# Optimization experiments

Hardware: AMD Instinct MI355X
Metric: run time of the kernel (lower is better)

Reference implementation:

```python
import jax, jax.numpy as jnp
import numpy as np

HEADS = 6
WSIZE = 8
SHIFTS = 4
EPS = 1e-5


def conv1x1(x, w, b=None):
    # x: (B,C,H,W), w: (O,C)
    y = jnp.einsum('bchw,oc->bohw', x, w)
    if b is not None:
        y = y + b[None, :, None, None]
    return y


def spatial_shift(x):
    # ShiftConv2d1 depthwise fixed-kernel conv == per-group spatial shift with zero pad
    C = x.shape[1]
    g = C // 5
    x0, x1, x2, x3, x4 = (x[:, :g], x[:, g:2 * g], x[:, 2 * g:3 * g],
                          x[:, 3 * g:4 * g], x[:, 4 * g:])
    left = jnp.pad(x0[:, :, :, 1:], ((0, 0), (0, 0), (0, 0), (0, 1)))   # kernel (1,2)
    right = jnp.pad(x1[:, :, :, :-1], ((0, 0), (0, 0), (0, 0), (1, 0)))  # kernel (1,0)
    up = jnp.pad(x2[:, :, 1:, :], ((0, 0), (0, 0), (0, 1), (0, 0)))      # kernel (2,1)
    down = jnp.pad(x3[:, :, :-1, :], ((0, 0), (0, 0), (1, 0), (0, 0)))   # kernel (0,1)
    return jnp.concatenate([left, right, up, down, x4], axis=1)


def window_attn(xb, ws, heads, shifts):
    # xb: (B, 2*heads*c, H, W); self-similarity attention q@q^T (no separate K, no scaling)
    if shifts > 0:
        xb = jnp.roll(xb, (-(ws // 2), -(ws // 2)), axis=(2, 3))
    b, c2, H, W = xb.shape
    cd = c2 // (2 * heads)
    nh, nw = H // ws, W // ws
    t = xb.reshape(b, 2, heads, cd, nh, ws, nw, ws)
    t = t.transpose(1, 0, 4, 6, 2, 5, 7, 3).reshape(2, b * nh * nw, heads, ws * ws, cd)
    q, v = t[0], t[1]
    atn = jax.nn.softmax(jnp.einsum('whnc,whmc->whnm', q, q), axis=-1)
    o = jnp.einsum('whnm,whmc->whnc', atn, v)
    o = o.reshape(b, nh, nw, heads, ws, ws, cd)
    o = o.transpose(0, 3, 6, 1, 4, 2, 5).reshape(b, heads * cd, H, W)
    if shifts > 0:
        o = jnp.roll(o, (ws // 2, ws // 2), axis=(2, 3))
    return o


def setup_inputs() -> dict:
    key = jax.random.key(0)
    ks = jax.random.split(key, 8)
    B, C, H, W = 2, 180, 256, 256
    s = 0.05
    return {
        'x': jax.random.normal(ks[0], (B, C, H, W), jnp.float32),
        'w0': jax.random.normal(ks[1], (2 * C, C), jnp.float32) * s,
        'b0': jnp.zeros((2 * C,), jnp.float32),
        'w1': jax.random.normal(ks[2], (C, 2 * C), jnp.float32) * s,
        'b1': jnp.zeros((C,), jnp.float32),
        'w_in': jax.random.normal(ks[3], (2 * C, C), jnp.float32) * s,
        'b_in': jnp.zeros((2 * C,), jnp.float32),
        'bn_g': jnp.ones((2 * C,), jnp.float32),
        'bn_b': jnp.zeros((2 * C,), jnp.float32),
        'w_out': jax.random.normal(ks[4], (C, C), jnp.float32) * s,
        'b_out': jnp.zeros((C,), jnp.float32),
    }


def reference(x, w0, b0, w1, b1, w_in, b_in, bn_g, bn_b, w_out, b_out):
    # --- LFE (shift-conv FFN), exp_ratio=2, relu ---
    y = conv1x1(spatial_shift(x), w0, b0)
    y = jax.nn.relu(y)
    y = conv1x1(spatial_shift(y), w1, b1)
    x = y + x
    # --- GMSA (3 parallel shifted-window self-similarity attentions) ---
    z = conv1x1(x, w_in, b_in)
    mu = z.mean(axis=(0, 2, 3), keepdims=True)
    var = z.var(axis=(0, 2, 3), keepdims=True)  # biased, matching BN training forward
    z = (z - mu) / jnp.sqrt(var + EPS) * bn_g[None, :, None, None] + bn_b[None, :, None, None]
    cs = z.shape[1] // 3
    sizes = [WSIZE // 4, WSIZE // 2, WSIZE]
    outs = [window_attn(z[:, i * cs:(i + 1) * cs], sizes[i], HEADS, SHIFTS)
            for i in range(3)]
    out = conv1x1(jnp.concatenate(outs, axis=1), w_out, b_out)
    return out + x
```

## Files before the change

### kernel.cpp

```cpp
#include <hip/hip_runtime.h>
#include <hip/hip_bf16.h>

#define HWSZ 65536
#define NPIX 131072

typedef unsigned short u16;
typedef __bf16 bf16x8 __attribute__((ext_vector_type(8)));
typedef float f32x4 __attribute__((ext_vector_type(4)));
typedef unsigned short u16x2 __attribute__((ext_vector_type(2)));
typedef unsigned short u16x4 __attribute__((ext_vector_type(4)));
typedef unsigned short u16x8 __attribute__((ext_vector_type(8)));
typedef unsigned short u16x8u __attribute__((ext_vector_type(8), aligned(4)));

__device__ inline u16 f2bf(float f) {
    unsigned int x = __builtin_bit_cast(unsigned int, f);
    unsigned int r = x + 0x7FFFu + ((x >> 16) & 1u);
    return (u16)(r >> 16);
}
__device__ inline float bf2f(u16 u) {
    unsigned int x = ((unsigned int)u) << 16;
    return __builtin_bit_cast(float, x);
}

__global__ __launch_bounds__(256) void prep_w(
    const float* __restrict__ w0, const float* __restrict__ w1,
    const float* __restrict__ wi, const float* __restrict__ wo,
    u16* __restrict__ W0p, u16* __restrict__ W1p,
    u16* __restrict__ Wip, u16* __restrict__ Wop)
{
    const int i = blockIdx.x * 256 + threadIdx.x;
    {
        const int r = i / 192, c = i % 192;
        const bool ok = (r < 360) && (c < 180);
        W0p[i] = ok ? f2bf(w0[r * 180 + c]) : (u16)0;
        Wip[i] = ok ? f2bf(wi[r * 180 + c]) : (u16)0;
    }
    {
        const int r = i / 384, c = i % 384;
        W1p[i] = (r < 180 && c < 360) ? f2bf(w1[r * 360 + c]) : (u16)0;
    }
    if (i < 36864) {
        const int r = i / 192, c = i % 192;
        Wop[i] = (r < 180 && c < 180) ? f2bf(wo[r * 180 + c]) : (u16)0;
    }
}

template<int CI, int G, int INM, int XSTR, bool RELU, bool BNPART>
__global__ __launch_bounds__(512) void conv_v14(
    const void* __restrict__ Xv, const u16* __restrict__ Wp,
    const float* __restrict__ bias, u16* __restrict__ Yh,
    float* __restrict__ part)
{
    constexpr int CI_PAD = ((CI + 31) / 32) * 32;
    constexpr int NSTEP  = CI_PAD / 32;
    constexpr int LDK    = 40;

    __shared__ u16 Xt[2][64 * LDK];

    const int tid = threadIdx.x;
    const int p0   = blockIdx.x << 6;
    const int b    = p0 >> 16;
    const int pix0 = p0 & 65535;
    const int h    = pix0 >> 8;
    const int w0c  = pix0 & 255;
    const int lane = tid & 63, wid = tid >> 6;
    const int lr = lane & 15, lg = lane >> 4;
    const int co_wave = wid * 48;

    const float* Xf = (const float*)Xv + (size_t)b * CI * HWSZ;
    const u16*   Xh = (const u16*)Xv;

    const int xn  = tid & 63;
    const int k4a = tid >> 6;

    auto loadX = [&](int kt, u16x4& r) {
        const int c0 = kt + k4a * 4;
        u16x4 v = {0, 0, 0, 0};
        if (c0 < CI) {
            int dh = 0, dw = 0;
            if (G > 0) {
                const int g = c0 / G;
                if      (g == 0) dw = 1;
                else if (g == 1) dw = -1;
                else if (g == 2) dh = 1;
                else if (g == 3) dh = -1;
            }
            const int hh = h + dh;
            const int wp = w0c + xn + dw;
            if (hh >= 0 && hh < 256 && wp >= 0 && wp < 256) {
                if constexpr (INM == 1) {
                    v = *(const u16x4*)&Xh[(size_t)((b << 16) | (hh << 8) | wp) * XSTR + c0];
                } else {
                    const float* xs = Xf + (size_t)c0 * HWSZ + hh * 256 + wp;
                    #pragma unroll
                    for (int j = 0; j < 4; ++j) v[j] = f2bf(xs[(size_t)j * HWSZ]);
                }
            }
        }
        r = v;
    };

    auto loadW = [&](int kt, bf16x8 (&a)[3]) {
        #pragma unroll
        for (int mf = 0; mf < 3; ++mf)
            a[mf] = *(const bf16x8*)&Wp[(size_t)(co_wave + mf * 16 + lr) * CI_PAD + kt + lg * 8];
    };

    auto writeLDS = [&](u16x4& r, int buf) {
        *(u16x4*)&Xt[buf][xn * LDK + k4a * 4] = r;
    };

    f32x4 acc[3][4] = {};
    u16x4 raw[2];
    bf16x8 af[2][3];

    loadX(0, raw[0]);
    loadW(0, af[0]);
    writeLDS(raw[0], 0);

    #pragma unroll
    for (int s = 0; s < NSTEP; ++s) {
        const int cur = s & 1, nxt = cur ^ 1;
        __syncthreads();
        if (s + 1 < NSTEP) {
            loadX((s + 1) * 32, raw[nxt]);
            loadW((s + 1) * 32, af[nxt]);
        }
        bf16x8 bfr[4];
        #pragma unroll
        for (int nf = 0; nf < 4; ++nf)
            bfr[nf] = *(const bf16x8*)&Xt[cur][(nf * 16 + lr) * LDK + lg * 8];
        #pragma unroll
        for (int mf = 0; mf < 3; ++mf)
            #pragma unroll
            for (int nf = 0; nf < 4; ++nf)
                acc[mf][nf] = __builtin_amdgcn_mfma_f32_16x16x32_bf16(
                    af[cur][mf], bfr[nf], acc[mf][nf], 0, 0, 0);
        if (s + 1 < NSTEP) writeLDS(raw[nxt], nxt);
    }

    float bsum[3][4] = {}, bsq[3][4] = {};
    #pragma unroll
    for (int mf = 0; mf < 3; ++mf) {
        const int co_b = co_wave + mf * 16 + lg * 4;
        if (co_b >= 360) continue;
        #pragma unroll
        for (int nf = 0; nf < 4; ++nf) {
            const size_t pg = (size_t)p0 + nf * 16 + lr;
            u16x4 o;
            #pragma unroll
            for (int r = 0; r < 4; ++r) {
                float v = acc[mf][nf][r] + bias[co_b + r];
                if (RELU) v = fmaxf(v, 0.f);
                o[r] = f2bf(v);
                if (BNPART) {
                    const float vr = bf2f(o[r]);
                    bsum[mf][r] += vr;
                    bsq[mf][r]  += vr * vr;
                }
            }
            *(u16x4*)&Yh[pg * 360 + co_b] = o;
        }
    }

    if (BNPART) {
        #pragma unroll
        for (int mf = 0; mf < 3; ++mf)
            #pragma unroll
            for (int r = 0; r < 4; ++r) {
                #pragma unroll
                for (int m = 1; m < 16; m <<= 1) {
                    bsum[mf][r] += __shfl_xor(bsum[mf][r], m, 64);
                    bsq[mf][r]  += __shfl_xor(bsq[mf][r],  m, 64);
                }
            }
        if (lr == 0) {
            float* pb = part + (size_t)blockIdx.x * 768;
            #pragma unroll
            for (int mf = 0; mf < 3; ++mf) {
                const int co_b = co_wave + mf * 16 + lg * 4;
                if (co_b >= 360) continue;
                f32x4 s4, q4;
                #pragma unroll
                for (int r = 0; r < 4; ++r) { s4[r] = bsum[mf][r]; q4[r] = bsq[mf][r]; }
                *(f32x4*)&pb[co_b]       = s4;
                *(f32x4*)&pb[384 + co_b] = q4;
            }
        }
    }
}

__global__ __launch_bounds__(256) void bn_fin2(const float* __restrict__ part,
                                               const float* __restrict__ g,
                                               const float* __restrict__ bb,
                                               float* __restrict__ sc,
                                               float* __restrict__ sh)
{
    const int c = blockIdx.x;
    const int t = threadIdx.x;
    float s = 0.f, q = 0.f;
    for (int k = t; k < 2048; k += 256) {
        s += part[(size_t)k * 768 + c];
        q += part[(size_t)k * 768 + 384 + c];
    }
    for (int m = 32; m; m >>= 1) {
        s += __shfl_xor(s, m, 64);
        q += __shfl_xor(q, m, 64);
    }
    __shared__ float rs[4], rq[4];
    if ((t & 63) == 0) { rs[t >> 6] = s; rq[t >> 6] = q; }
    __syncthreads();
    if (t == 0) {
        const float su = rs[0] + rs[1] + rs[2] + rs[3];
        const float sq = rq[0] + rq[1] + rq[2] + rq[3];
        const float invN = 1.f / (float)NPIX;
        const float mean = su * invN;
        const float var  = sq * invN - mean * mean;
        const float istd = 1.f / sqrtf(var + 1e-5f);
        const float scv  = g[c] * istd;
        sc[c] = scv;
        sh[c] = bb[c] - mean * scv;
    }
}

template<int CI, int CO, int G, int XSTR, bool RELU, int RES, int OUTM, int OSTR, bool COSPLIT>
__global__ __launch_bounds__(256) void conv_v10(
    const u16* __restrict__ Xh, const u16* __restrict__ Wp,
    const float* __restrict__ bias, const void* __restrict__ Rv,
    void* __restrict__ Yv)
{
    constexpr int CI_PAD = ((CI + 31) / 32) * 32;
    constexpr int NSTEP  = CI_PAD / 32;

    __shared__ u16 Xt[2][256 * 8];

    const int tid = threadIdx.x;
    const int bid = blockIdx.x;
    int px_tile, co0;
    if (COSPLIT) {
        co0     = ((bid >> 3) & 1) * 192;
        px_tile = ((bid >> 4) << 3) | (bid & 7);
    } else {
        co0 = blockIdx.y * 192; px_tile = bid;
    }
    const int p0   = px_tile << 6;
    const int b    = p0 >> 16;
    const int pix0 = p0 & 65535;
    const int h    = pix0 >> 8;
    const int w0c  = pix0 & 255;
    const int lane = tid & 63, wid = tid >> 6;
    const int lr = lane & 15, lg = lane >> 4;
    const int co_wave = co0 + wid * 48;

    const int sg  = (wid << 6) | lane;
    const int spx = sg >> 2;
    const int khp = sg & 3;
    const int kh  = khp ^ ((spx >> 1) & 3);

    auto stage = [&](int kt, int buf) {
        const int c0 = kt + kh * 8;
        u16* ldst_lane = &Xt[buf][sg * 8];
        int dh = 0, dw = 0; bool uni = true;
        if (G > 0) {
            const int g0 = c0 / G;
            uni = (g0 == (c0 + 7) / G);
            if      (g0 == 0) dw = 1;
            else if (g0 == 1) dw = -1;
            else if (g0 == 2) dh = 1;
            else if (g0 == 3) dh = -1;
        }
        const int hh = h + dh, wp = w0c + spx + dw;
        const bool pxok = (hh >= 0 && hh < 256 && wp >= 0 && wp < 256);
        if (c0 < CI && uni && pxok) {
            const u16* src = &Xh[(size_t)((b << 16) | (hh << 8) | wp) * XSTR + c0];
            u16* wbase = &Xt[buf][(wid << 6) * 8];
            __builtin_amdgcn_global_load_lds(
                (const __attribute__((address_space(1))) unsigned int*)src,
                (__attribute__((address_space(3))) unsigned int*)wbase, 16, 0, 0);
        } else {
            u16x8 t = {0, 0, 0, 0, 0, 0, 0, 0};
            if (c0 < CI && pxok) {
                #pragma unroll
                for (int j = 0; j < 8; ++j) {
                    const int c = c0 + j;
                    if (c < CI) {
                        int dh2 = 0, dw2 = 0;
                        if (G > 0) {
                            const int g = c / G;
                            if      (g == 0) dw2 = 1;
                            else if (g == 1) dw2 = -1;
                            else if (g == 2) dh2 = 1;
                            else if (g == 3) dh2 = -1;
                        }
                        const int h2 = h + dh2, w2 = w0c + spx + dw2;
                        if (h2 >= 0 && h2 < 256 && w2 >= 0 && w2 < 256)
                            t[j] = Xh[(size_t)((b << 16) | (h2 << 8) | w2) * XSTR + c];
                    }
                }
            }
            *(u16x8*)ldst_lane = t;
        }
    };

    auto loadW = [&](int kt, bf16x8 (&a)[3]) {
        #pragma unroll
        for (int mf = 0; mf < 3; ++mf)
            a[mf] = *(const bf16x8*)&Wp[(size_t)(co_wave + mf * 16 + lr) * CI_PAD + kt + lg * 8];
    };

    f32x4 acc[3][4] = {};
    bf16x8 af[2][3];

    stage(0, 0);
    loadW(0, af[0]);
    __syncthreads();

    #pragma unroll
    for (int s = 0; s < NSTEP; ++s) {
        const int cur = s & 1, nxt = cur ^ 1;
        if (s + 1 < NSTEP) {
            stage((s + 1) * 32, nxt);
            loadW((s + 1) * 32, af[nxt]);
        }
        bf16x8 bfr[4];
        #pragma unroll
        for (int nf = 0; nf < 4; ++nf) {
            const int pxr = nf * 16 + lr;
            const int kpp = lg ^ ((pxr >> 1) & 3);
            bfr[nf] = *(const bf16x8*)&Xt[cur][pxr * 32 + kpp * 8];
        }
        #pragma unroll
        for (int mf = 0; mf < 3; ++mf)
            #pragma unroll
            for (int nf = 0; nf < 4; ++nf)
                acc[mf][nf] = __builtin_amdgcn_mfma_f32_16x16x32_bf16(
                    af[cur][mf], bfr[nf], acc[mf][nf], 0, 0, 0);
        __syncthreads();
    }

    const float* Rf = (const float*)Rv;
    const u16*   Rh = (const u16*)Rv;
    #pragma unroll
    for (int mf = 0; mf < 3; ++mf) {
        const int co_b = co_wave + mf * 16 + lg * 4;
        if (co_b >= CO) continue;
        #pragma unroll
        for (int nf = 0; nf < 4; ++nf) {
            const int pl = pix0 + nf * 16 + lr;
            const size_t pg = (size_t)p0 + nf * 16 + lr;
            float v[4];
            #pragma unroll
            for (int r = 0; r < 4; ++r) {
                v[r] = acc[mf][nf][r] + bias[co_b + r];
                if (RELU) v[r] = fmaxf(v[r], 0.f);
            }
            if (RES == 1) {
                #pragma unroll
                for (int r = 0; r < 4; ++r)
                    v[r] += Rf[((size_t)(b * CO + co_b + r)) * HWSZ + pl];
            }
            if (RES == 2) {
                u16x4 rr = *(const u16x4*)&Rh[pg * 180 + co_b];
                #pragma unroll
                for (int r = 0; r < 4; ++r) v[r] += bf2f(rr[r]);
            }
            if (OUTM == 1) {
                u16x4 o;
                #pragma unroll
                for (int r = 0; r < 4; ++r) o[r] = f2bf(v[r]);
                *(u16x4*)&((u16*)Yv)[pg * OSTR + co_b] = o;
            } else {
                #pragma unroll
                for (int r = 0; r < 4; ++r)
                    ((float*)Yv)[((size_t)(b * CO + co_b + r)) * HWSZ + pl] = v[r];
            }
        }
    }
}

template<int WS>
__global__ __launch_bounds__(256) void attn_v3(
    const u16* __restrict__ zt, const float* __restrict__ scale,
    const float* __restrict__ shiftc, u16* __restrict__ ot, int chunk)
{
    constexpr int NP  = WS * WS;
    constexpr int GPB = 256 / NP;
    constexpr int SH  = WS / 2;
    constexpr int NW  = 256 / WS;

    __shared__ float qs[256 * 12];
    __shared__ float vs[256 * 12];
    __shared__ float scs[120], shs[120];

    const int tid = threadIdx.x;
    if (tid < 120) {
        scs[tid] = scale[chunk * 120 + tid];
        shs[tid] = shiftc[chunk * 120 + tid];
    }

    const int lg  = tid / NP;
    const int n   = tid % NP;
    const int gidx = blockIdx.x * GPB + lg;

    const int head = gidx % 6;
    const int win  = gidx / 6;
    const int wcol = win % NW;
    const int tmp  = win / NW;
    const int wrow = tmp % NW;
    const int b    = tmp / NW;

    const int i = n / WS, j = n % WS;
    const int hh = (wrow * WS + i + SH) & 255;
    const int ww = (wcol * WS + j + SH) & 255;
    const size_t zrow = (size_t)((b << 16) | (hh << 8) | ww) * 360;

    const int cq = chunk * 120 + head * 10;
    const int cl = head * 10;

    u16x8u q8 = *(const u16x8u*)&zt[zrow + cq];
    u16x2  q2 = *(const u16x2*)&zt[zrow + cq + 8];
    u16x8u v8 = *(const u16x8u*)&zt[zrow + cq + 60];
    u16x2  v2 = *(const u16x2*)&zt[zrow + cq + 68];
    __syncthreads();

    float q[10];
    float* qrow = &qs[tid * 12];
    float* vrow = &vs[tid * 12];
    #pragma unroll
    for (int c = 0; c < 8; ++c) {
        q[c] = bf2f(q8[c]) * scs[cl + c] + shs[cl + c];
        qrow[c] = q[c];
        vrow[c] = bf2f(v8[c]) * scs[60 + cl + c] + shs[60 + cl + c];
    }
    q[8] = bf2f(q2[0]) * scs[cl + 8] + shs[cl + 8];
    q[9] = bf2f(q2[1]) * scs[cl + 9] + shs[cl + 9];
    qrow[8] = q[8]; qrow[9] = q[9];
    vrow[8] = bf2f(v2[0]) * scs[60 + cl + 8] + shs[60 + cl + 8];
    vrow[9] = bf2f(v2[1]) * scs[60 + cl + 9] + shs[60 + cl + 9];
    qrow[10] = 0.f; qrow[11] = 0.f;
    vrow[10] = 0.f; vrow[11] = 0.f;
    __syncthreads();

    const float* qg = &qs[(lg * NP) * 12];
    const float* vg = &vs[(lg * NP) * 12];

    float mx = -1e30f;
    for (int m = 0; m < NP; ++m) {
        f32x4 a0 = *(const f32x4*)&qg[m * 12];
        f32x4 a1 = *(const f32x4*)&qg[m * 12 + 4];
        f32x4 a2 = *(const f32x4*)&qg[m * 12 + 8];
        float d = q[0]*a0[0] + q[1]*a0[1] + q[2]*a0[2] + q[3]*a0[3]
                + q[4]*a1[0] + q[5]*a1[1] + q[6]*a1[2] + q[7]*a1[3]
                + q[8]*a2[0] + q[9]*a2[1];
        mx = fmaxf(mx, d);
    }
    float s = 0.f;
    float o[10] = {};
    for (int m = 0; m < NP; ++m) {
        f32x4 a0 = *(const f32x4*)&qg[m * 12];
        f32x4 a1 = *(const f32x4*)&qg[m * 12 + 4];
        f32x4 a2 = *(const f32x4*)&qg[m * 12 + 8];
        float d = q[0]*a0[0] + q[1]*a0[1] + q[2]*a0[2] + q[3]*a0[3]
                + q[4]*a1[0] + q[5]*a1[1] + q[6]*a1[2] + q[7]*a1[3]
                + q[8]*a2[0] + q[9]*a2[1];
        float e = __expf(d - mx);
        s += e;
        f32x4 b0 = *(const f32x4*)&vg[m * 12];
        f32x4 b1 = *(const f32x4*)&vg[m * 12 + 4];
        f32x4 b2 = *(const f32x4*)&vg[m * 12 + 8];
        o[0] += e * b0[0]; o[1] += e * b0[1]; o[2] += e * b0[2]; o[3] += e * b0[3];
        o[4] += e * b1[0]; o[5] += e * b1[1]; o[6] += e * b1[2]; o[7] += e * b1[3];
        o[8] += e * b2[0]; o[9] += e * b2[1];
    }
    const float inv = 1.f / s;
    u16* orow = ot + (size_t)((b << 16) | (hh << 8) | ww) * 180 + chunk * 60 + head * 10;
    u16x8u o8;
    #pragma unroll
    for (int c = 0; c < 8; ++c) o8[c] = f2bf(o[c] * inv);
    u16x2 o2;
    o2[0] = f2bf(o[8] * inv);
    o2[1] = f2bf(o[9] * inv);
    *(u16x8u*)&orow[0] = o8;
    *(u16x2*)&orow[8]  = o2;
}

extern "C" void kernel_launch(void* const* d_in, const int* in_sizes, int n_in,
                              void* d_out, int out_size, void* d_ws, size_t ws_size,
                              hipStream_t stream)
{
    const float* x     = (const float*)d_in[0];
    const float* w0    = (const float*)d_in[1];
    const float* b0    = (const float*)d_in[2];
    const float* w1    = (const float*)d_in[3];
    const float* b1    = (const float*)d_in[4];
    const float* w_in  = (const float*)d_in[5];
    const float* b_in  = (const float*)d_in[6];
    const float* bn_g  = (const float*)d_in[7];
    const float* bn_b  = (const float*)d_in[8];
    const float* w_out = (const float*)d_in[9];
    const float* b_out = (const float*)d_in[10];
    float* out = (float*)d_out;

    u16* y   = (u16*)d_ws;
    u16* x1b = y   + (size_t)NPIX * 360;
    u16* ot  = x1b + (size_t)NPIX * 180;
    u16* W0p = ot  + (size_t)NPIX * 180;
    u16* Wip = W0p + 384 * 192;
    u16* W1p = Wip + 384 * 192;
    u16* Wop = W1p + 192 * 384;
    float* part   = (float*)(Wop + 192 * 192);
    float* scale  = part + (size_t)2048 * 768;
    float* shiftc = scale + 360;
    u16* zt = y;

    dim3 blk(256);
    dim3 blk8(512);

    prep_w<<<dim3(288), blk, 0, stream>>>(w0, w1, w_in, w_out, W0p, W1p, Wip, Wop);

    conv_v14<180, 36, 0, 0,   true,  false>
        <<<dim3(2048), blk8, 0, stream>>>(x, W0p, b0, y, nullptr);
    conv_v10<360, 180, 72, 360, false, 1, 1, 180, false>
        <<<dim3(2048, 1), blk, 0, stream>>>(y, W1p, b1, x, x1b);
    conv_v14<180, 0,  1, 180, false, true >
        <<<dim3(2048), blk8, 0, stream>>>(x1b, Wip, b_in, zt, part);
    bn_fin2<<<dim3(360), blk, 0, stream>>>(part, bn_g, bn_b, scale, shiftc);
    attn_v3<2><<<dim3(3072), blk, 0, stream>>>(zt, scale, shiftc, ot, 0);
    attn_v3<4><<<dim3(3072), blk, 0, stream>>>(zt, scale, shiftc, ot, 1);
    attn_v3<8><<<dim3(3072), blk, 0, stream>>>(zt, scale, shiftc, ot, 2);
    conv_v10<180, 180, 0,  180, false, 2, 0, 0, false>
        <<<dim3(2048, 1), blk, 0, stream>>>(ot, Wop, b_out, x1b, out);
}
```

Before: 387.0 us.

## Replace conv_v10 with 512-thread 128-pixel tile conv using register-staged LDS loads

Adds conv_v15, a 1x1-conv GEMM kernel with 512 threads covering 128 pixels per block (two pixel halves by four output-channel waves). It replaces the two conv_v10 launches (the second LFE conv and the output projection). Each weight fragment is now reused across twice as many pixels and the grid is halved. X tiles are loaded with 4-element vector global reads into registers, then written to a padded LDS tile after the MFMAs, instead of using global_load_lds with an XOR swizzle and per-element fallback. The risks are more registers per thread, narrower 8-byte global loads, and possible LDS bank conflicts from the 40-element padded stride.

```diff
diff --git a/kernel.cpp b/kernel.cpp
--- a/kernel.cpp
+++ b/kernel.cpp
@@ -190,6 +190,133 @@
     }
 }
 
+template<int CI, int G, int XSTR, int RES, int OUTM, int OSTR>
+__global__ __launch_bounds__(512) void conv_v15(
+    const u16* __restrict__ Xh, const u16* __restrict__ Wp,
+    const float* __restrict__ bias, const void* __restrict__ Rv,
+    void* __restrict__ Yv)
+{
+    constexpr int CI_PAD = ((CI + 31) / 32) * 32;
+    constexpr int NSTEP  = CI_PAD / 32;
+    constexpr int LDK    = 40;
+
+    __shared__ u16 Xt[2][128 * LDK];
+
+    const int tid = threadIdx.x;
+    const int p0   = blockIdx.x << 7;
+    const int b    = p0 >> 16;
+    const int pix0 = p0 & 65535;
+    const int h    = pix0 >> 8;
+    const int w0c  = pix0 & 255;
+    const int lane = tid & 63, wid = tid >> 6;
+    const int lr = lane & 15, lg = lane >> 4;
+    const int ph  = wid >> 2;
+    const int co_wave = (wid & 3) * 48;
+
+    const int xn  = tid & 127;
+    const int k4a = tid >> 7;
+
+    auto loadX = [&](int kt, u16x4 (&r)[2]) {
+        #pragma unroll
+        for (int it = 0; it < 2; ++it) {
+            const int c0 = kt + (k4a + it * 4) * 4;
+            u16x4 v = {0, 0, 0, 0};
+            if (c0 < CI) {
+                int dh = 0, dw = 0;
+                if (G > 0) {
+                    const int g = c0 / G;
+                    if      (g == 0) dw = 1;
+                    else if (g == 1) dw = -1;
+                    else if (g == 2) dh = 1;
+                    else if (g == 3) dh = -1;
+                }
+                const int hh = h + dh;
+                const int wp = w0c + xn + dw;
+                if (hh >= 0 && hh < 256 && wp >= 0 && wp < 256)
+                    v = *(const u16x4*)&Xh[(size_t)((b << 16) | (hh << 8) | wp) * XSTR + c0];
+            }
+            r[it] = v;
+        }
+    };
+
+    auto loadW = [&](int kt, bf16x8 (&a)[3]) {
+        #pragma unroll
+        for (int mf = 0; mf < 3; ++mf)
+            a[mf] = *(const bf16x8*)&Wp[(size_t)(co_wave + mf * 16 + lr) * CI_PAD + kt + lg * 8];
+    };
+
+    auto writeLDS = [&](u16x4 (&r)[2], int buf) {
+        *(u16x4*)&Xt[buf][xn * LDK + k4a * 4]       = r[0];
+        *(u16x4*)&Xt[buf][xn * LDK + (k4a + 4) * 4] = r[1];
+    };
+
+    f32x4 acc[3][4] = {};
+    u16x4 raw[2][2];
+    bf16x8 af[2][3];
+
+    loadX(0, raw[0]);
+    loadW(0, af[0]);
+    writeLDS(raw[0], 0);
+
+    #pragma unroll
+    for (int s = 0; s < NSTEP; ++s) {
+        const int cur = s & 1, nxt = cur ^ 1;
+        __syncthreads();
+        if (s + 1 < NSTEP) {
+            loadX((s + 1) * 32, raw[nxt]);
+            loadW((s + 1) * 32, af[nxt]);
+        }
+        bf16x8 bfr[4];
+        #pragma unroll
+        for (int nf = 0; nf < 4; ++nf)
+            bfr[nf] = *(const bf16x8*)&Xt[cur][(ph * 64 + nf * 16 + lr) * LDK + lg * 8];
+        #pragma unroll
+        for (int mf = 0; mf < 3; ++mf)
+            #pragma unroll
+            for (int nf = 0; nf < 4; ++nf)
+                acc[mf][nf] = __builtin_amdgcn_mfma_f32_16x16x32_bf16(
+                    af[cur][mf], bfr[nf], acc[mf][nf], 0, 0, 0);
+        if (s + 1 < NSTEP) writeLDS(raw[nxt], nxt);
+    }
+
+    const float* Rf = (const float*)Rv;
+    const u16*   Rh = (const u16*)Rv;
+    #pragma unroll
+    for (int mf = 0; mf < 3; ++mf) {
+        const int co_b = co_wave + mf * 16 + lg * 4;
+        if (co_b >= 180) continue;
+        #pragma unroll
+        for (int nf = 0; nf < 4; ++nf) {
+            const int pl = pix0 + ph * 64 + nf * 16 + lr;
+            const size_t pg = (size_t)p0 + ph * 64 + nf * 16 + lr;
+            float v[4];
+            #pragma unroll
+            for (int r = 0; r < 4; ++r)
+                v[r] = acc[mf][nf][r] + bias[co_b + r];
+            if (RES == 1) {
+                #pragma unroll
+                for (int r = 0; r < 4; ++r)
+                    v[r] += Rf[((size_t)(b * 180 + co_b + r)) * HWSZ + pl];
+            }
+            if (RES == 2) {
+                u16x4 rr = *(const u16x4*)&Rh[pg * 180 + co_b];
+                #pragma unroll
+                for (int r = 0; r < 4; ++r) v[r] += bf2f(rr[r]);
+            }
+            if (OUTM == 1) {
+                u16x4 o;
+                #pragma unroll
+                for (int r = 0; r < 4; ++r) o[r] = f2bf(v[r]);
+                *(u16x4*)&((u16*)Yv)[pg * OSTR + co_b] = o;
+            } else {
+                #pragma unroll
+                for (int r = 0; r < 4; ++r)
+                    ((float*)Yv)[((size_t)(b * 180 + co_b + r)) * HWSZ + pl] = v[r];
+            }
+        }
+    }
+}
+
 __global__ __launch_bounds__(256) void bn_fin2(const float* __restrict__ part,
                                                const float* __restrict__ g,
                                                const float* __restrict__ bb,
@@ -220,161 +347,6 @@
         const float scv  = g[c] * istd;
         sc[c] = scv;
         sh[c] = bb[c] - mean * scv;
-    }
-}
-
-template<int CI, int CO, int G, int XSTR, bool RELU, int RES, int OUTM, int OSTR, bool COSPLIT>
-__global__ __launch_bounds__(256) void conv_v10(
-    const u16* __restrict__ Xh, const u16* __restrict__ Wp,
-    const float* __restrict__ bias, const void* __restrict__ Rv,
-    void* __restrict__ Yv)
-{
-    constexpr int CI_PAD = ((CI + 31) / 32) * 32;
-    constexpr int NSTEP  = CI_PAD / 32;
-
-    __shared__ u16 Xt[2][256 * 8];
-
-    const int tid = threadIdx.x;
-    const int bid = blockIdx.x;
-    int px_tile, co0;
-    if (COSPLIT) {
-        co0     = ((bid >> 3) & 1) * 192;
-        px_tile = ((bid >> 4) << 3) | (bid & 7);
-    } else {
-        co0 = blockIdx.y * 192; px_tile = bid;
-    }
-    const int p0   = px_tile << 6;
-    const int b    = p0 >> 16;
-    const int pix0 = p0 & 65535;
-    const int h    = pix0 >> 8;
-    const int w0c  = pix0 & 255;
-    const int lane = tid & 63, wid = tid >> 6;
-    const int lr = lane & 15, lg = lane >> 4;
-    const int co_wave = co0 + wid * 48;
-
-    const int sg  = (wid << 6) | lane;
-    const int spx = sg >> 2;
-    const int khp = sg & 3;
-    const int kh  = khp ^ ((spx >> 1) & 3);
-
-    auto stage = [&](int kt, int buf) {
-        const int c0 = kt + kh * 8;
-        u16* ldst_lane = &Xt[buf][sg * 8];
-        int dh = 0, dw = 0; bool uni = true;
-        if (G > 0) {
-            const int g0 = c0 / G;
-            uni = (g0 == (c0 + 7) / G);
-            if      (g0 == 0) dw = 1;
-            else if (g0 == 1) dw = -1;
-            else if (g0 == 2) dh = 1;
-            else if (g0 == 3) dh = -1;
-        }
-        const int hh = h + dh, wp = w0c + spx + dw;
-        const bool pxok = (hh >= 0 && hh < 256 && wp >= 0 && wp < 256);
-        if (c0 < CI && uni && pxok) {
-            const u16* src = &Xh[(size_t)((b << 16) | (hh << 8) | wp) * XSTR + c0];
-            u16* wbase = &Xt[buf][(wid << 6) * 8];
-            __builtin_amdgcn_global_load_lds(
-                (const __attribute__((address_space(1))) unsigned int*)src,
-                (__attribute__((address_space(3))) unsigned int*)wbase, 16, 0, 0);
-        } else {
-            u16x8 t = {0, 0, 0, 0, 0, 0, 0, 0};
-            if (c0 < CI && pxok) {
-                #pragma unroll
-                for (int j = 0; j < 8; ++j) {
-                    const int c = c0 + j;
-                    if (c < CI) {
-                        int dh2 = 0, dw2 = 0;
-                        if (G > 0) {
-                            const int g = c / G;
-                            if      (g == 0) dw2 = 1;
-                            else if (g == 1) dw2 = -1;
-                            else if (g == 2) dh2 = 1;
-                            else if (g == 3) dh2 = -1;
-                        }
-                        const int h2 = h + dh2, w2 = w0c + spx + dw2;
-                        if (h2 >= 0 && h2 < 256 && w2 >= 0 && w2 < 256)
-                            t[j] = Xh[(size_t)((b << 16) | (h2 << 8) | w2) * XSTR + c];
-                    }
-                }
-            }
-            *(u16x8*)ldst_lane = t;
-        }
-    };
-
-    auto loadW = [&](int kt, bf16x8 (&a)[3]) {
-        #pragma unroll
-        for (int mf = 0; mf < 3; ++mf)
-            a[mf] = *(const bf16x8*)&Wp[(size_t)(co_wave + mf * 16 + lr) * CI_PAD + kt + lg * 8];
-    };
-
-    f32x4 acc[3][4] = {};
-    bf16x8 af[2][3];
-
-    stage(0, 0);
-    loadW(0, af[0]);
-    __syncthreads();
-
-    #pragma unroll
-    for (int s = 0; s < NSTEP; ++s) {
-        const int cur = s & 1, nxt = cur ^ 1;
-        if (s + 1 < NSTEP) {
-            stage((s + 1) * 32, nxt);
-            loadW((s + 1) * 32, af[nxt]);
-        }
-        bf16x8 bfr[4];
-        #pragma unroll
-        for (int nf = 0; nf < 4; ++nf) {
-            const int pxr = nf * 16 + lr;
-            const int kpp = lg ^ ((pxr >> 1) & 3);
-            bfr[nf] = *(const bf16x8*)&Xt[cur][pxr * 32 + kpp * 8];
-        }
-        #pragma unroll
-        for (int mf = 0; mf < 3; ++mf)
-            #pragma unroll
-            for (int nf = 0; nf < 4; ++nf)
-                acc[mf][nf] = __builtin_amdgcn_mfma_f32_16x16x32_bf16(
-                    af[cur][mf], bfr[nf], acc[mf][nf], 0, 0, 0);
-        __syncthreads();
-    }
-
-    const float* Rf = (const float*)Rv;
-    const u16*   Rh = (const u16*)Rv;
-    #pragma unroll
-    for (int mf = 0; mf < 3; ++mf) {
-        const int co_b = co_wave + mf * 16 + lg * 4;
-        if (co_b >= CO) continue;
-        #pragma unroll
-        for (int nf = 0; nf < 4; ++nf) {
-            const int pl = pix0 + nf * 16 + lr;
-            const size_t pg = (size_t)p0 + nf * 16 + lr;
-            float v[4];
-            #pragma unroll
-            for (int r = 0; r < 4; ++r) {
-                v[r] = acc[mf][nf][r] + bias[co_b + r];
-                if (RELU) v[r] = fmaxf(v[r], 0.f);
-            }
-            if (RES == 1) {
-                #pragma unroll
-                for (int r = 0; r < 4; ++r)
-                    v[r] += Rf[((size_t)(b * CO + co_b + r)) * HWSZ + pl];
-            }
-            if (RES == 2) {
-                u16x4 rr = *(const u16x4*)&Rh[pg * 180 + co_b];
-                #pragma unroll
-                for (int r = 0; r < 4; ++r) v[r] += bf2f(rr[r]);
-            }
-            if (OUTM == 1) {
-                u16x4 o;
-                #pragma unroll
-                for (int r = 0; r < 4; ++r) o[r] = f2bf(v[r]);
-                *(u16x4*)&((u16*)Yv)[pg * OSTR + co_b] = o;
-            } else {
-                #pragma unroll
-                for (int r = 0; r < 4; ++r)
-                    ((float*)Yv)[((size_t)(b * CO + co_b + r)) * HWSZ + pl] = v[r];
-            }
-        }
     }
 }
 
@@ -520,14 +492,14 @@
 
     conv_v14<180, 36, 0, 0,   true,  false>
         <<<dim3(2048), blk8, 0, stream>>>(x, W0p, b0, y, nullptr);
-    conv_v10<360, 180, 72, 360, false, 1, 1, 180, false>
-        <<<dim3(2048, 1), blk, 0, stream>>>(y, W1p, b1, x, x1b);
+    conv_v15<360, 72, 360, 1, 1, 180>
+        <<<dim3(1024), blk8, 0, stream>>>(y, W1p, b1, x, x1b);
     conv_v14<180, 0,  1, 180, false, true >
         <<<dim3(2048), blk8, 0, stream>>>(x1b, Wip, b_in, zt, part);
     bn_fin2<<<dim3(360), blk, 0, stream>>>(part, bn_g, bn_b, scale, shiftc);
     attn_v3<2><<<dim3(3072), blk, 0, stream>>>(zt, scale, shiftc, ot, 0);
     attn_v3<4><<<dim3(3072), blk, 0, stream>>>(zt, scale, shiftc, ot, 1);
     attn_v3<8><<<dim3(3072), blk, 0, stream>>>(zt, scale, shiftc, ot, 2);
-    conv_v10<180, 180, 0,  180, false, 2, 0, 0, false>
-        <<<dim3(2048, 1), blk, 0, stream>>>(ot, Wop, b_out, x1b, out);
-}
+    conv_v15<180, 0,  180, 2, 0, 0>
+        <<<dim3(1024), blk8, 0, stream>>>(ot, Wop, b_out, x1b, out);
+}
```

Result: slower. 402.2 us (+3.9%).
